# Performance work log

Measured on AMD Instinct MI355X. Metric: run time of the kernel, lower is better.

The kernel has to match this reference:

```python
import jax, jax.numpy as jnp
import numpy as np

N_NODE = 100_000
N_EDGE = 1_000_000
N_QUERY = 256
N_REL = 200  # embedding table has 2*N_REL+1 = 401 rows
IN_DIM = 64
OUT_DIM = 64
ATTN_DIM = 64


def setup_inputs() -> dict:
    key = jax.random.key(0)
    ks = jax.random.split(key, 12)
    r_idx = jax.random.randint(ks[0], (N_EDGE,), 0, N_QUERY)
    rel = jax.random.randint(ks[1], (N_EDGE,), 0, 2 * N_REL + 1)
    sub = jax.random.randint(ks[2], (N_EDGE,), 0, N_NODE)
    obj = jax.random.randint(ks[3], (N_EDGE,), 0, N_NODE)
    zeros = jnp.zeros((N_EDGE,), dtype=jnp.int32)
    # columns: [r_idx, _, rel, _, sub, obj] matching edges[:,0],[:,2],[:,4],[:,5]
    edges = jnp.stack([r_idx, zeros, rel, zeros, sub, obj], axis=1)
    return {
        "q_sub": jax.random.randint(ks[4], (N_QUERY,), 0, N_NODE),
        "q_rel": jax.random.randint(ks[5], (N_QUERY,), 0, 2 * N_REL + 1),
        "hidden": jax.random.normal(ks[6], (N_NODE, IN_DIM), dtype=jnp.float32),
        "edges": edges,
        "n_node": N_NODE,
        "rela_embed": jax.random.normal(ks[7], (2 * N_REL + 1, IN_DIM), dtype=jnp.float32) * 0.1,
        "Ws": jax.random.normal(ks[8], (IN_DIM, ATTN_DIM), dtype=jnp.float32) * (IN_DIM ** -0.5),
        "Wr": jax.random.normal(ks[9], (IN_DIM, ATTN_DIM), dtype=jnp.float32) * (IN_DIM ** -0.5),
        "Wqr": jax.random.normal(ks[10], (IN_DIM, ATTN_DIM), dtype=jnp.float32) * (IN_DIM ** -0.5),
        "Wqr_b": jnp.zeros((ATTN_DIM,), dtype=jnp.float32),
        "w_alpha_w": jax.random.normal(ks[11], (ATTN_DIM, 1), dtype=jnp.float32) * (ATTN_DIM ** -0.5),
        "w_alpha_b": jnp.zeros((1,), dtype=jnp.float32),
        "W_h": jax.random.normal(jax.random.fold_in(key, 99), (IN_DIM, OUT_DIM), dtype=jnp.float32) * (IN_DIM ** -0.5),
    }


def reference(q_sub, q_rel, hidden, edges, n_node, rela_embed, Ws, Wr, Wqr,
              Wqr_b, w_alpha_w, w_alpha_b, W_h):
    sub = edges[:, 4]
    rel = edges[:, 2]
    obj = edges[:, 5]
    r_idx = edges[:, 0]

    hs = hidden[sub]                    # [E, in_dim] gather
    hr = rela_embed[rel]                # [E, in_dim]
    h_qr = rela_embed[q_rel][r_idx]     # [E, in_dim]

    message = hs + hr                   # [E, in_dim]

    attn = jax.nn.relu(hs @ Ws + hr @ Wr + (h_qr @ Wqr + Wqr_b))  # [E, attn_dim]
    alpha_temp = attn @ w_alpha_w + w_alpha_b                      # [E, 1]
    alpha = jax.nn.sigmoid(alpha_temp)                             # [E, 1]

    message = alpha * message
    message_agg = jax.ops.segment_sum(message, obj, num_segments=n_node)  # [n_node, in_dim]
    hidden_new = message_agg @ W_h      # act is identity (default)
    return hidden_new, alpha, message, obj, alpha_temp
```

## Files before the change

### kernel.cpp

```cpp
#include <hip/hip_runtime.h>
#include <hip/hip_bf16.h>
#include <hip/hip_fp16.h>
#include <cstddef>


typedef float    f32x4 __attribute__((ext_vector_type(4)));
typedef _Float16 f16x4 __attribute__((ext_vector_type(4)));

static __device__ __forceinline__ void nt_store4(float* p, float4 v) {
    f32x4 t = {v.x, v.y, v.z, v.w};
    __builtin_nontemporal_store(t, (f32x4*)p);
}
#define NT_STORE(p, v) __builtin_nontemporal_store((v), (p))

__global__ void fused_pre_kernel(const float* __restrict__ hidden,
                                 const float* __restrict__ Ws,
                                 _Float16* __restrict__ packed, int nnode,
                                 const float* __restrict__ rela,
                                 const float* __restrict__ Wr,
                                 const float* __restrict__ Wqr,
                                 const float* __restrict__ Wqr_b,
                                 const int* __restrict__ q_rel,
                                 float* __restrict__ Br,
                                 float* __restrict__ Cq, int nrel, int nq,
                                 _Float16* __restrict__ agg,
                                 int mmB, int relB, int zB) {
    __shared__ float W1[64][64];
    __shared__ float W2[64][64];
    int bid = blockIdx.x;
    int tid = threadIdx.x;

    if (bid < mmB) {
        for (int i = tid; i < 4096; i += 256) W1[i >> 6][i & 63] = Ws[i];
        __syncthreads();
        int col = tid & 63, r4 = tid >> 6;
        for (long row = (long)bid * 4 + r4; row < nnode; row += (long)mmB * 4) {
            float xv  = hidden[row * 64 + col];
            float acc = 0.0f;
#pragma unroll
            for (int k = 0; k < 64; ++k)
                acc = fmaf(__shfl(xv, k, 64), W1[k][col], acc);
            packed[row * 128 + col]      = (_Float16)xv;
            packed[row * 128 + 64 + col] = (_Float16)acc;
        }
    } else if (bid < mmB + relB) {
        for (int i = tid; i < 4096; i += 256) {
            W1[i >> 6][i & 63] = Wr[i];
            W2[i >> 6][i & 63] = Wqr[i];
        }
        __syncthreads();
        int col = tid & 63, r4 = tid >> 6;
        int row = (bid - mmB) * 4 + r4;
        int total = nrel + nq;
        if (row < total) {
            if (row < nrel) {
                float xv  = rela[(size_t)row * 64 + col];
                float acc = 0.0f;
#pragma unroll
                for (int k = 0; k < 64; ++k)
                    acc = fmaf(__shfl(xv, k, 64), W1[k][col], acc);
                Br[(size_t)row * 64 + col] = acc;
            } else {
                int q  = row - nrel;
                int rr = q_rel[q];
                float xv  = rela[(size_t)rr * 64 + col];
                float acc = Wqr_b[col];
#pragma unroll
                for (int k = 0; k < 64; ++k)
                    acc = fmaf(__shfl(xv, k, 64), W2[k][col], acc);
                Cq[(size_t)q * 64 + col] = acc;
            }
        }
    } else {
        size_t n16 = (size_t)nnode * 8;
        size_t i = (size_t)(bid - mmB - relB) * 256 + tid;
        size_t stride = (size_t)zB * 256;
        f32x4 z = {0.f, 0.f, 0.f, 0.f};
        for (; i < n16; i += stride)
            __builtin_nontemporal_store(z, (f32x4*)agg + i);
    }
}

__global__ void edge_kernel(const int* __restrict__ edges,
                            const _Float16* __restrict__ packed,
                            const float* __restrict__ rela,
                            const float* __restrict__ Br,
                            const float* __restrict__ Cq,
                            const float* __restrict__ w_alpha_w,
                            const float* __restrict__ w_alpha_b,
                            _Float16* __restrict__ agg,
                            float* __restrict__ out_alpha,
                            float* __restrict__ out_message,
                            float* __restrict__ out_obj,
                            float* __restrict__ out_alpha_temp,
                            int nedge) {
    int tid  = threadIdx.x;
    int lane = tid & 63;
    int g    = lane >> 4;
    int s    = lane & 15;
    long e0  = ((long)blockIdx.x * 4 + (tid >> 6)) * 4;
    if (e0 >= nedge) return;
    long e   = e0 + g;
    bool valid = (e < nedge);

    int md = 0;
    long mbase = e0 * 6;
    if (lane < 24 && (mbase + lane) < (long)nedge * 6) md = edges[mbase + lane];
    int r_idx = __shfl(md, g * 6 + 0, 64);
    int rel   = __shfl(md, g * 6 + 2, 64);
    int sub   = __shfl(md, g * 6 + 4, 64);
    int obj   = __shfl(md, g * 6 + 5, 64);
    if (!valid) { r_idx = 0; rel = 0; sub = 0; obj = 0; }

    const f16x4 hh = *(const f16x4*)(packed + (size_t)sub * 128 + s * 4);
    const f16x4 hw = *(const f16x4*)(packed + (size_t)sub * 128 + 64 + s * 4);
    const float4 b4 = *(const float4*)(Br   + (size_t)rel  * 64 + s * 4);
    const float4 c4 = *(const float4*)(Cq   + (size_t)r_idx* 64 + s * 4);
    const float4 rv = *(const float4*)(rela   + (size_t)rel * 64 + s * 4);
    const float4 wa = *(const float4*)(w_alpha_w + s * 4);

    float4 a4;
    a4.x = fmaxf((float)hw[0] + b4.x + c4.x, 0.0f);
    a4.y = fmaxf((float)hw[1] + b4.y + c4.y, 0.0f);
    a4.z = fmaxf((float)hw[2] + b4.z + c4.z, 0.0f);
    a4.w = fmaxf((float)hw[3] + b4.w + c4.w, 0.0f);

    float part = a4.x * wa.x + a4.y * wa.y + a4.z * wa.z + a4.w * wa.w;
    part += __shfl_xor(part, 1, 64);
    part += __shfl_xor(part, 2, 64);
    part += __shfl_xor(part, 4, 64);
    part += __shfl_xor(part, 8, 64);

    float at    = part + w_alpha_b[0];
    float alpha = 1.0f / (1.0f + __expf(-at));

    float4 m4;
    m4.x = alpha * ((float)hh[0] + rv.x);
    m4.y = alpha * ((float)hh[1] + rv.y);
    m4.z = alpha * ((float)hh[2] + rv.z);
    m4.w = alpha * ((float)hh[3] + rv.w);

    if (valid) {
        nt_store4(out_message + e * 64 + s * 4, m4);
        if (s == 0) {
            NT_STORE(&out_alpha[e], alpha);
            NT_STORE(&out_obj[e], (float)obj);
            NT_STORE(&out_alpha_temp[e], at);
        }
    }

    int h = lane & 31;
#pragma unroll
    for (int i = 0; i < 2; ++i) {
        int k = i * 2 + (lane >> 5);
        if (e0 + k < nedge) {
            int srcl = k * 16 + (h >> 1);
            float xk = __shfl(m4.x, srcl, 64);
            float yk = __shfl(m4.y, srcl, 64);
            float zk = __shfl(m4.z, srcl, 64);
            float wk = __shfl(m4.w, srcl, 64);
            __half2 v = (h & 1) ? __floats2half2_rn(zk, wk)
                                : __floats2half2_rn(xk, yk);
            int ok = __shfl(obj, k * 16, 64);
            unsafeAtomicAdd((__half2*)(agg + (size_t)ok * 64) + h, v);
        }
    }
}

__global__ void matmul64_f16_kernel(const _Float16* __restrict__ X,
                                    const float* __restrict__ W,
                                    float* __restrict__ Y, int nrows) {
    __shared__ float Wl[64][64];
    int tid = threadIdx.x;
    for (int i = tid; i < 4096; i += 256) Wl[i >> 6][i & 63] = W[i];
    __syncthreads();
    int col = tid & 63;
    int r4  = tid >> 6;
    for (long row = (long)blockIdx.x * 4 + r4; row < nrows;
         row += (long)gridDim.x * 4) {
        float xv  = (float)X[row * 64 + col];
        float acc = 0.0f;
#pragma unroll
        for (int k = 0; k < 64; ++k)
            acc = fmaf(__shfl(xv, k, 64), Wl[k][col], acc);
        NT_STORE(&Y[row * 64 + col], acc);
    }
}

extern "C" void kernel_launch(void* const* d_in, const int* in_sizes, int n_in,
                              void* d_out, int out_size, void* d_ws, size_t ws_size,
                              hipStream_t stream) {
    const int*   q_rel     = (const int*)d_in[1];
    const float* hidden    = (const float*)d_in[2];
    const int*   edges     = (const int*)d_in[3];
    const float* rela      = (const float*)d_in[5];
    const float* Ws        = (const float*)d_in[6];
    const float* Wr        = (const float*)d_in[7];
    const float* Wqr       = (const float*)d_in[8];
    const float* Wqr_b     = (const float*)d_in[9];
    const float* w_alpha_w = (const float*)d_in[10];
    const float* w_alpha_b = (const float*)d_in[11];
    const float* W_h       = (const float*)d_in[12];

    const int n_node = in_sizes[2] / 64;
    const int n_edge = in_sizes[3] / 6;
    const int n_rel  = in_sizes[5] / 64;
    const int n_q    = in_sizes[1];

    float* out            = (float*)d_out;
    float* out_hidden_new = out;
    float* out_alpha      = out + (size_t)n_node * 64;
    float* out_message    = out_alpha + n_edge;
    float* out_obj        = out_message + (size_t)n_edge * 64;
    float* out_alpha_temp = out_obj + n_edge;

    _Float16* packed = (_Float16*)d_ws;
    _Float16* agg    = packed + (size_t)n_node * 128;
    float*    Br     = (float*)(agg + (size_t)n_node * 64);
    float*    Cq     = Br + (size_t)n_rel * 64;

    const int mmB  = 2048;
    const int relB = (n_rel + n_q + 3) / 4;
    const int zB   = 512;
    fused_pre_kernel<<<mmB + relB + zB, 256, 0, stream>>>(
        hidden, Ws, packed, n_node,
        rela, Wr, Wqr, Wqr_b, q_rel, Br, Cq, n_rel, n_q,
        agg, mmB, relB, zB);

    {
        int grid = (n_edge + 15) / 16;
        edge_kernel<<<grid, 256, 0, stream>>>(edges, packed, rela, Br, Cq,
                                              w_alpha_w, w_alpha_b, agg,
                                              out_alpha, out_message, out_obj,
                                              out_alpha_temp, n_edge);
    }

    matmul64_f16_kernel<<<2048, 256, 0, stream>>>(agg, W_h, out_hidden_new,
                                                  n_node);
}
```

Measured before the change: 274.9 us.

## Process eight edges per wave with fp16 relation tables and LDS-staged atomics

The edge kernel now assigns 8 lanes per edge with 8-wide fp16 loads, so each wave handles 8 edges instead of 4 and the grid is halved. The Br, Cq and relation-embedding tables are precomputed in fp16 to halve their gather bytes. The message shuffle redistribution before the half2 atomics is replaced with staging through shared memory plus a block barrier. This trades extra fp16 rounding in the attention inputs and a __syncthreads for fewer, wider memory transactions.

```diff
diff --git a/kernel.cpp b/kernel.cpp
--- a/kernel.cpp
+++ b/kernel.cpp
@@ -5,12 +5,8 @@
 
 
 typedef float    f32x4 __attribute__((ext_vector_type(4)));
-typedef _Float16 f16x4 __attribute__((ext_vector_type(4)));
-
-static __device__ __forceinline__ void nt_store4(float* p, float4 v) {
-    f32x4 t = {v.x, v.y, v.z, v.w};
-    __builtin_nontemporal_store(t, (f32x4*)p);
-}
+typedef _Float16 f16x8 __attribute__((ext_vector_type(8)));
+
 #define NT_STORE(p, v) __builtin_nontemporal_store((v), (p))
 
 __global__ void fused_pre_kernel(const float* __restrict__ hidden,
@@ -21,8 +17,10 @@
                                  const float* __restrict__ Wqr,
                                  const float* __restrict__ Wqr_b,
                                  const int* __restrict__ q_rel,
-                                 float* __restrict__ Br,
-                                 float* __restrict__ Cq, int nrel, int nq,
+                                 _Float16* __restrict__ Br16,
+                                 _Float16* __restrict__ Cq16,
+                                 _Float16* __restrict__ rela16,
+                                 int nrel, int nq,
                                  _Float16* __restrict__ agg,
                                  int mmB, int relB, int zB) {
     __shared__ float W1[64][64];
@@ -59,7 +57,8 @@
 #pragma unroll
                 for (int k = 0; k < 64; ++k)
                     acc = fmaf(__shfl(xv, k, 64), W1[k][col], acc);
-                Br[(size_t)row * 64 + col] = acc;
+                Br16[(size_t)row * 64 + col]   = (_Float16)acc;
+                rela16[(size_t)row * 64 + col] = (_Float16)xv;
             } else {
                 int q  = row - nrel;
                 int rr = q_rel[q];
@@ -68,7 +67,7 @@
 #pragma unroll
                 for (int k = 0; k < 64; ++k)
                     acc = fmaf(__shfl(xv, k, 64), W2[k][col], acc);
-                Cq[(size_t)q * 64 + col] = acc;
+                Cq16[(size_t)q * 64 + col] = (_Float16)acc;
             }
         }
     } else {
@@ -83,9 +82,9 @@
 
 __global__ void edge_kernel(const int* __restrict__ edges,
                             const _Float16* __restrict__ packed,
-                            const float* __restrict__ rela,
-                            const float* __restrict__ Br,
-                            const float* __restrict__ Cq,
+                            const _Float16* __restrict__ rela16,
+                            const _Float16* __restrict__ Br16,
+                            const _Float16* __restrict__ Cq16,
                             const float* __restrict__ w_alpha_w,
                             const float* __restrict__ w_alpha_b,
                             _Float16* __restrict__ agg,
@@ -94,54 +93,58 @@
                             float* __restrict__ out_obj,
                             float* __restrict__ out_alpha_temp,
                             int nedge) {
+    __shared__ __align__(16) _Float16 sm[4][8][64];
     int tid  = threadIdx.x;
+    int wv   = tid >> 6;
     int lane = tid & 63;
-    int g    = lane >> 4;
-    int s    = lane & 15;
-    long e0  = ((long)blockIdx.x * 4 + (tid >> 6)) * 4;
-    if (e0 >= nedge) return;
+    int g    = lane >> 3;
+    int s    = lane & 7;
+    long e0  = ((long)blockIdx.x * 4 + wv) * 8;
+    if ((long)blockIdx.x * 32 >= nedge) return;
     long e   = e0 + g;
     bool valid = (e < nedge);
 
     int md = 0;
     long mbase = e0 * 6;
-    if (lane < 24 && (mbase + lane) < (long)nedge * 6) md = edges[mbase + lane];
+    if (lane < 48 && (mbase + lane) < (long)nedge * 6) md = edges[mbase + lane];
     int r_idx = __shfl(md, g * 6 + 0, 64);
     int rel   = __shfl(md, g * 6 + 2, 64);
     int sub   = __shfl(md, g * 6 + 4, 64);
     int obj   = __shfl(md, g * 6 + 5, 64);
     if (!valid) { r_idx = 0; rel = 0; sub = 0; obj = 0; }
 
-    const f16x4 hh = *(const f16x4*)(packed + (size_t)sub * 128 + s * 4);
-    const f16x4 hw = *(const f16x4*)(packed + (size_t)sub * 128 + 64 + s * 4);
-    const float4 b4 = *(const float4*)(Br   + (size_t)rel  * 64 + s * 4);
-    const float4 c4 = *(const float4*)(Cq   + (size_t)r_idx* 64 + s * 4);
-    const float4 rv = *(const float4*)(rela   + (size_t)rel * 64 + s * 4);
-    const float4 wa = *(const float4*)(w_alpha_w + s * 4);
-
-    float4 a4;
-    a4.x = fmaxf((float)hw[0] + b4.x + c4.x, 0.0f);
-    a4.y = fmaxf((float)hw[1] + b4.y + c4.y, 0.0f);
-    a4.z = fmaxf((float)hw[2] + b4.z + c4.z, 0.0f);
-    a4.w = fmaxf((float)hw[3] + b4.w + c4.w, 0.0f);
-
-    float part = a4.x * wa.x + a4.y * wa.y + a4.z * wa.z + a4.w * wa.w;
-    part += __shfl_xor(part, 1, 64);
-    part += __shfl_xor(part, 2, 64);
-    part += __shfl_xor(part, 4, 64);
-    part += __shfl_xor(part, 8, 64);
-
-    float at    = part + w_alpha_b[0];
+    const f16x8 hh = *(const f16x8*)(packed + (size_t)sub * 128 + s * 8);
+    const f16x8 hw = *(const f16x8*)(packed + (size_t)sub * 128 + 64 + s * 8);
+    const f16x8 br = *(const f16x8*)(Br16   + (size_t)rel   * 64 + s * 8);
+    const f16x8 cq = *(const f16x8*)(Cq16   + (size_t)r_idx * 64 + s * 8);
+    const f16x8 rv = *(const f16x8*)(rela16 + (size_t)rel   * 64 + s * 8);
+    const f32x4 wa0 = *(const f32x4*)(w_alpha_w + s * 8);
+    const f32x4 wa1 = *(const f32x4*)(w_alpha_w + s * 8 + 4);
+
+    float dot = 0.0f;
+#pragma unroll
+    for (int j = 0; j < 8; ++j) {
+        float a  = fmaxf((float)hw[j] + (float)br[j] + (float)cq[j], 0.0f);
+        float wj = (j < 4) ? wa0[j] : wa1[j - 4];
+        dot = fmaf(a, wj, dot);
+    }
+    dot += __shfl_xor(dot, 1, 64);
+    dot += __shfl_xor(dot, 2, 64);
+    dot += __shfl_xor(dot, 4, 64);
+
+    float at    = dot + w_alpha_b[0];
     float alpha = 1.0f / (1.0f + __expf(-at));
 
-    float4 m4;
-    m4.x = alpha * ((float)hh[0] + rv.x);
-    m4.y = alpha * ((float)hh[1] + rv.y);
-    m4.z = alpha * ((float)hh[2] + rv.z);
-    m4.w = alpha * ((float)hh[3] + rv.w);
+    float m[8];
+#pragma unroll
+    for (int j = 0; j < 8; ++j)
+        m[j] = alpha * ((float)hh[j] + (float)rv[j]);
 
     if (valid) {
-        nt_store4(out_message + e * 64 + s * 4, m4);
+        f32x4 m0 = {m[0], m[1], m[2], m[3]};
+        f32x4 m1 = {m[4], m[5], m[6], m[7]};
+        __builtin_nontemporal_store(m0, (f32x4*)(out_message + e * 64 + s * 8));
+        __builtin_nontemporal_store(m1, (f32x4*)(out_message + e * 64 + s * 8 + 4));
         if (s == 0) {
             NT_STORE(&out_alpha[e], alpha);
             NT_STORE(&out_obj[e], (float)obj);
@@ -149,19 +152,18 @@
         }
     }
 
-    int h = lane & 31;
-#pragma unroll
-    for (int i = 0; i < 2; ++i) {
-        int k = i * 2 + (lane >> 5);
+    f16x8 mh;
+#pragma unroll
+    for (int j = 0; j < 8; ++j) mh[j] = (_Float16)m[j];
+    *(f16x8*)&sm[wv][g][s * 8] = mh;
+    __syncthreads();
+#pragma unroll
+    for (int i = 0; i < 4; ++i) {
+        int k = 2 * i + (lane >> 5);
+        int h = lane & 31;
         if (e0 + k < nedge) {
-            int srcl = k * 16 + (h >> 1);
-            float xk = __shfl(m4.x, srcl, 64);
-            float yk = __shfl(m4.y, srcl, 64);
-            float zk = __shfl(m4.z, srcl, 64);
-            float wk = __shfl(m4.w, srcl, 64);
-            __half2 v = (h & 1) ? __floats2half2_rn(zk, wk)
-                                : __floats2half2_rn(xk, yk);
-            int ok = __shfl(obj, k * 16, 64);
+            __half2 v = *(__half2*)&sm[wv][k][h * 2];
+            int ok = __shfl(obj, k * 8, 64);
             unsafeAtomicAdd((__half2*)(agg + (size_t)ok * 64) + h, v);
         }
     }
@@ -216,20 +218,21 @@
 
     _Float16* packed = (_Float16*)d_ws;
     _Float16* agg    = packed + (size_t)n_node * 128;
-    float*    Br     = (float*)(agg + (size_t)n_node * 64);
-    float*    Cq     = Br + (size_t)n_rel * 64;
+    _Float16* Br16   = agg + (size_t)n_node * 64;
+    _Float16* Cq16   = Br16 + (size_t)n_rel * 64;
+    _Float16* rela16 = Cq16 + (size_t)n_q * 64;
 
     const int mmB  = 2048;
     const int relB = (n_rel + n_q + 3) / 4;
     const int zB   = 512;
     fused_pre_kernel<<<mmB + relB + zB, 256, 0, stream>>>(
         hidden, Ws, packed, n_node,
-        rela, Wr, Wqr, Wqr_b, q_rel, Br, Cq, n_rel, n_q,
+        rela, Wr, Wqr, Wqr_b, q_rel, Br16, Cq16, rela16, n_rel, n_q,
         agg, mmB, relB, zB);
 
     {
-        int grid = (n_edge + 15) / 16;
-        edge_kernel<<<grid, 256, 0, stream>>>(edges, packed, rela, Br, Cq,
+        int grid = (n_edge + 31) / 32;
+        edge_kernel<<<grid, 256, 0, stream>>>(edges, packed, rela16, Br16, Cq16,
                                               w_alpha_w, w_alpha_b, agg,
                                               out_alpha, out_message, out_obj,
                                               out_alpha_temp, n_edge);
```

After: 266.8 us. 1.03x faster.
